# Kernel optimization log

Measured on AMD Instinct MI355X. Metric: run time of the kernel, lower is better.

Reference implementation:

```python
import jax, jax.numpy as jnp
import numpy as np

B, S, D_IN, D_OUT, NUM_LAYERS = 128, 64, 2048, 2048, 64

def setup_inputs() -> dict:
    key = jax.random.key(0)
    k1, k2, k3 = jax.random.split(key, 3)
    x = jax.random.normal(k1, (B, S, D_IN), dtype=jnp.float32)
    weight = jax.random.normal(k2, (NUM_LAYERS, D_OUT, D_IN), dtype=jnp.float32)
    layer_idx = jax.random.randint(k3, (S,), 0, NUM_LAYERS, dtype=jnp.int32)
    return {"x": x, "weight": weight, "layer_idx": layer_idx}

def reference(x, weight, layer_idx):
    # x: [B, S, D_in]; weight: [L, D_out, D_in]; layer_idx: [S] ints in [0, L)
    # Per position s: out[:, s, :] = x[:, s, :] @ weight[layer_idx[s]].T
    w_sel = weight[layer_idx]                      # [S, D_out, D_in] gather
    out = jnp.einsum('bsd,sod->bso', x, w_sel)     # batched per-position GEMMs
    return out
```

## Files before the change

### kernel.cpp

```cpp
#include <hip/hip_runtime.h>
#include <hip/hip_bf16.h>

#define B_DIM 128
#define S_DIM 64
#define DIN   2048
#define DOUT  2048
#define NLAYERS 64

#define BM 128
#define BN 64
#define BK 64
#define NK (DIN / BK)
#define TPP (DOUT / BN)
#define NTILES (S_DIM * TPP)
#define NXCD 8
#define APADE 2048

typedef __bf16 bf16_t;
typedef __attribute__((ext_vector_type(8))) bf16_t bf16x8;
typedef __attribute__((ext_vector_type(4))) float f32x4;

__global__ void rank_sort(const int* __restrict__ layer_idx, int* __restrict__ perm) {
    __shared__ int L[S_DIM];
    const int s = threadIdx.x;
    L[s] = layer_idx[s];
    __syncthreads();
    const int mine = L[s];
    int rank = 0;
    #pragma unroll
    for (int t = 0; t < S_DIM; ++t) {
        const int lt = L[t];
        rank += (lt < mine || (lt == mine && t < s)) ? 1 : 0;
    }
    perm[rank] = s;
}

__global__ void convert_x(const float* __restrict__ x, bf16_t* __restrict__ x16) {
    const size_t i = ((size_t)blockIdx.x * 256 + threadIdx.x) * 8;
    f32x4 a = *(const f32x4*)(x + i);
    f32x4 b = *(const f32x4*)(x + i + 4);
    bf16x8 v;
    #pragma unroll
    for (int j = 0; j < 4; ++j) { v[j] = (bf16_t)a[j]; v[j + 4] = (bf16_t)b[j]; }
    *(bf16x8*)(x16 + i) = v;
}

template <bool XBF16>
__launch_bounds__(256, 2)
__global__ void flex_linear_gemm(const float* __restrict__ x,
                                 const bf16_t* __restrict__ x16,
                                 const float* __restrict__ w,
                                 const int* __restrict__ layer_idx,
                                 const int* __restrict__ perm,
                                 float* __restrict__ out) {
    __shared__ bf16_t Alds[2][BM * BK + APADE];
    __shared__ bf16_t Blds[2][BN * BK];

    const int orig = blockIdx.x;
    const int xcd  = orig & (NXCD - 1);
    const int slot = orig >> 3;
    const int tile = xcd * (NTILES / NXCD) + slot;
    const int yy   = tile / TPP;
    const int nb   = tile % TPP;

    const int s  = perm[yy];
    const int layer = layer_idx[s];

    const float* Bg = w + (size_t)layer * (size_t)(DOUT * DIN) + (size_t)(nb * BN) * DIN;

    const int tid  = threadIdx.x;
    const int lane = tid & 63;
    const int wave = tid >> 6;
    const int wr = (wave >> 1) * 64;
    const int wc = (wave & 1) * 32;
    const int lrow = lane & 15;
    const int lk   = (lane >> 4) * 8;

    int offWA[4], offWB[2];
    const float*  pA[4];
    const bf16_t* pA16[4];
    const float*  pB[2];
    #pragma unroll
    for (int i = 0; i < 4; ++i) {
        const int c   = tid + 256 * i;
        const int row = c >> 3;
        const int kc8 = (c & 7) * 8;
        offWA[i] = (row * BK + kc8) ^ ((row & 7) << 3);
        const size_t aoff = (size_t)row * (S_DIM * DIN) + (size_t)s * DIN + kc8;
        pA[i]   = x   + aoff;
        pA16[i] = x16 + aoff;
    }
    #pragma unroll
    for (int i = 0; i < 2; ++i) {
        const int c   = tid + 256 * i;
        const int row = c >> 3;
        const int kc8 = (c & 7) * 8;
        offWB[i] = (row * BK + kc8) ^ ((row & 7) << 3);
        pB[i] = Bg + (size_t)row * DIN + kc8;
    }
    int offA[2][4], offB[2][2];
    #pragma unroll
    for (int kk = 0; kk < 2; ++kk) {
        #pragma unroll
        for (int m = 0; m < 4; ++m) {
            const int ra = wr + m * 16 + lrow;
            offA[kk][m] = (ra * BK + kk * 32 + lk) ^ ((ra & 7) << 3);
        }
        #pragma unroll
        for (int n = 0; n < 2; ++n) {
            const int rb = wc + n * 16 + lrow;
            offB[kk][n] = (rb * BK + kk * 32 + lk) ^ ((rb & 7) << 3);
        }
    }

    bf16x8 RA16[4];
    f32x4  RA[8];
    f32x4  RB[4];
    f32x4  acc[4][2] = {};

    auto issue = [&](int kb) {
        const int koff = kb * BK;
        #pragma unroll
        for (int i = 0; i < 4; ++i) {
            if constexpr (XBF16) {
                RA16[i] = *(const bf16x8*)(pA16[i] + koff);
            } else {
                const float* a = pA[i] + koff;
                RA[2 * i]     = *(const f32x4*)a;
                RA[2 * i + 1] = *(const f32x4*)(a + 4);
            }
        }
        #pragma unroll
        for (int i = 0; i < 2; ++i) {
            const float* b = pB[i] + koff;
            RB[2 * i]     = *(const f32x4*)b;
            RB[2 * i + 1] = *(const f32x4*)(b + 4);
        }
    };
    auto cvt_write = [&](int buf) {
        bf16_t* Al = &Alds[buf][0];
        bf16_t* Bl = &Blds[buf][0];
        #pragma unroll
        for (int i = 0; i < 4; ++i) {
            if constexpr (XBF16) {
                *(bf16x8*)&Al[offWA[i]] = RA16[i];
            } else {
                bf16x8 va;
                #pragma unroll
                for (int j = 0; j < 4; ++j) {
                    va[j]     = (bf16_t)RA[2 * i][j];
                    va[j + 4] = (bf16_t)RA[2 * i + 1][j];
                }
                *(bf16x8*)&Al[offWA[i]] = va;
            }
        }
        #pragma unroll
        for (int i = 0; i < 2; ++i) {
            bf16x8 vb;
            #pragma unroll
            for (int j = 0; j < 4; ++j) {
                vb[j]     = (bf16_t)RB[2 * i][j];
                vb[j + 4] = (bf16_t)RB[2 * i + 1][j];
            }
            *(bf16x8*)&Bl[offWB[i]] = vb;
        }
    };
    auto compute = [&](int buf) {
        const bf16_t* Al = &Alds[buf][0];
        const bf16_t* Bl = &Blds[buf][0];
        #pragma unroll
        for (int kk = 0; kk < 2; ++kk) {
            bf16x8 af[4], bfr[2];
            #pragma unroll
            for (int m = 0; m < 4; ++m) af[m]  = *(const bf16x8*)&Al[offA[kk][m]];
            #pragma unroll
            for (int n = 0; n < 2; ++n) bfr[n] = *(const bf16x8*)&Bl[offB[kk][n]];
            #pragma unroll
            for (int m = 0; m < 4; ++m)
                #pragma unroll
                for (int n = 0; n < 2; ++n)
                    acc[m][n] = __builtin_amdgcn_mfma_f32_16x16x32_bf16(af[m], bfr[n], acc[m][n], 0, 0, 0);
        }
    };

    issue(0);
    cvt_write(0);
    issue(1);
    for (int kb = 0; kb < NK - 1; ++kb) {
        __syncthreads();
        compute(kb & 1);
        cvt_write((kb + 1) & 1);
        if (kb + 2 < NK) issue(kb + 2);
    }
    __syncthreads();
    compute((NK - 1) & 1);

    float* Og = out + (size_t)s * DOUT + (size_t)(nb * BN);
    #pragma unroll
    for (int m = 0; m < 4; ++m) {
        const int rb = wr + m * 16 + (lane >> 4) * 4;
        #pragma unroll
        for (int r = 0; r < 4; ++r) {
            float* orow = Og + (size_t)(rb + r) * (S_DIM * DOUT);
            #pragma unroll
            for (int n = 0; n < 2; ++n)
                __builtin_nontemporal_store(acc[m][n][r], &orow[wc + n * 16 + (lane & 15)]);
        }
    }
}

extern "C" void kernel_launch(void* const* d_in, const int* in_sizes, int n_in,
                              void* d_out, int out_size, void* d_ws, size_t ws_size,
                              hipStream_t stream) {
    const float* x         = (const float*)d_in[0];
    const float* w         = (const float*)d_in[1];
    const int*   layer_idx = (const int*)d_in[2];
    float*       out       = (float*)d_out;

    int*    perm = (int*)d_ws;
    bf16_t* x16  = (bf16_t*)((char*)d_ws + 512);
    const size_t need = 512 + (size_t)B_DIM * S_DIM * DIN * sizeof(bf16_t);

    rank_sort<<<1, S_DIM, 0, stream>>>(layer_idx, perm);

    if (ws_size >= need) {
        convert_x<<<(B_DIM * S_DIM * DIN / 8) / 256, 256, 0, stream>>>(x, x16);
        flex_linear_gemm<true><<<NTILES, dim3(256), 0, stream>>>(x, x16, w, layer_idx, perm, out);
    } else {
        flex_linear_gemm<false><<<NTILES, dim3(256), 0, stream>>>(x, x16, w, layer_idx, perm, out);
    }
}
```

Baseline: 231.8 us.

## Fuse rank sort into conversion kernel and relax loop barrier to LDS-only wait

Merges the permutation sort into the x-conversion kernel to drop one kernel launch. Replaces __syncthreads in the GEMM main loop with an explicit lgkmcnt wait plus s_barrier, so in-flight global prefetches need not drain at each barrier. The LDS buffers are merged into one array with explicit offsets. The fallback path now runs the conversion kernel into the workspace even when it is too small, which could write out of bounds there.

```diff
diff --git a/kernel.cpp b/kernel.cpp
--- a/kernel.cpp
+++ b/kernel.cpp
@@ -14,28 +14,34 @@
 #define TPP (DOUT / BN)
 #define NTILES (S_DIM * TPP)
 #define NXCD 8
-#define APADE 2048
+
+#define LDS_A 8192
+#define LDS_B 4096
+#define LDS_ELEMS 28672
+#define A_OFF(b) ((b) * LDS_A)
+#define B_OFF(b) (2 * LDS_A + (b) * LDS_B)
 
 typedef __bf16 bf16_t;
 typedef __attribute__((ext_vector_type(8))) bf16_t bf16x8;
 typedef __attribute__((ext_vector_type(4))) float f32x4;
 
-__global__ void rank_sort(const int* __restrict__ layer_idx, int* __restrict__ perm) {
+__global__ void prep(const float* __restrict__ x, bf16_t* __restrict__ x16,
+                     const int* __restrict__ layer_idx, int* __restrict__ perm) {
     __shared__ int L[S_DIM];
-    const int s = threadIdx.x;
-    L[s] = layer_idx[s];
-    __syncthreads();
-    const int mine = L[s];
-    int rank = 0;
-    #pragma unroll
-    for (int t = 0; t < S_DIM; ++t) {
-        const int lt = L[t];
-        rank += (lt < mine || (lt == mine && t < s)) ? 1 : 0;
-    }
-    perm[rank] = s;
-}
-
-__global__ void convert_x(const float* __restrict__ x, bf16_t* __restrict__ x16) {
+    if (blockIdx.x == 0) {
+        if (threadIdx.x < S_DIM) L[threadIdx.x] = layer_idx[threadIdx.x];
+        __syncthreads();
+        if (threadIdx.x < S_DIM) {
+            const int s = threadIdx.x, mine = L[s];
+            int rank = 0;
+            #pragma unroll
+            for (int t = 0; t < S_DIM; ++t) {
+                const int lt = L[t];
+                rank += (lt < mine || (lt == mine && t < s)) ? 1 : 0;
+            }
+            perm[rank] = s;
+        }
+    }
     const size_t i = ((size_t)blockIdx.x * 256 + threadIdx.x) * 8;
     f32x4 a = *(const f32x4*)(x + i);
     f32x4 b = *(const f32x4*)(x + i + 4);
@@ -43,6 +49,14 @@
     #pragma unroll
     for (int j = 0; j < 4; ++j) { v[j] = (bf16_t)a[j]; v[j + 4] = (bf16_t)b[j]; }
     *(bf16x8*)(x16 + i) = v;
+}
+
+__device__ __forceinline__ void lgkm_barrier() {
+    __builtin_amdgcn_sched_barrier(0);
+    asm volatile("s_waitcnt lgkmcnt(0)" ::: "memory");
+    __builtin_amdgcn_sched_barrier(0);
+    __builtin_amdgcn_s_barrier();
+    __builtin_amdgcn_sched_barrier(0);
 }
 
 template <bool XBF16>
@@ -53,15 +67,14 @@
                                  const int* __restrict__ layer_idx,
                                  const int* __restrict__ perm,
                                  float* __restrict__ out) {
-    __shared__ bf16_t Alds[2][BM * BK + APADE];
-    __shared__ bf16_t Blds[2][BN * BK];
+    __shared__ bf16_t lds[LDS_ELEMS];
 
     const int orig = blockIdx.x;
     const int xcd  = orig & (NXCD - 1);
     const int slot = orig >> 3;
     const int tile = xcd * (NTILES / NXCD) + slot;
-    const int yy   = tile / TPP;
-    const int nb   = tile % TPP;
+    const int yy   = tile >> 5;
+    const int nb   = tile & 31;
 
     const int s  = perm[yy];
     const int layer = layer_idx[s];
@@ -138,8 +151,8 @@
         }
     };
     auto cvt_write = [&](int buf) {
-        bf16_t* Al = &Alds[buf][0];
-        bf16_t* Bl = &Blds[buf][0];
+        bf16_t* Al = &lds[A_OFF(buf)];
+        bf16_t* Bl = &lds[B_OFF(buf)];
         #pragma unroll
         for (int i = 0; i < 4; ++i) {
             if constexpr (XBF16) {
@@ -166,8 +179,8 @@
         }
     };
     auto compute = [&](int buf) {
-        const bf16_t* Al = &Alds[buf][0];
-        const bf16_t* Bl = &Blds[buf][0];
+        const bf16_t* Al = &lds[A_OFF(buf)];
+        const bf16_t* Bl = &lds[B_OFF(buf)];
         #pragma unroll
         for (int kk = 0; kk < 2; ++kk) {
             bf16x8 af[4], bfr[2];
@@ -186,14 +199,13 @@
     issue(0);
     cvt_write(0);
     issue(1);
-    for (int kb = 0; kb < NK - 1; ++kb) {
-        __syncthreads();
+    lgkm_barrier();
+    for (int kb = 0; kb < NK; ++kb) {
         compute(kb & 1);
-        cvt_write((kb + 1) & 1);
+        if (kb + 1 < NK) cvt_write((kb + 1) & 1);
         if (kb + 2 < NK) issue(kb + 2);
-    }
-    __syncthreads();
-    compute((NK - 1) & 1);
+        lgkm_barrier();
+    }
 
     float* Og = out + (size_t)s * DOUT + (size_t)(nb * BN);
     #pragma unroll
@@ -221,12 +233,11 @@
     bf16_t* x16  = (bf16_t*)((char*)d_ws + 512);
     const size_t need = 512 + (size_t)B_DIM * S_DIM * DIN * sizeof(bf16_t);
 
-    rank_sort<<<1, S_DIM, 0, stream>>>(layer_idx, perm);
-
     if (ws_size >= need) {
-        convert_x<<<(B_DIM * S_DIM * DIN / 8) / 256, 256, 0, stream>>>(x, x16);
+        prep<<<(B_DIM * S_DIM * DIN / 8) / 256, 256, 0, stream>>>(x, x16, layer_idx, perm);
         flex_linear_gemm<true><<<NTILES, dim3(256), 0, stream>>>(x, x16, w, layer_idx, perm, out);
     } else {
+        prep<<<(B_DIM * S_DIM * DIN / 8) / 256, 256, 0, stream>>>(x, x16, layer_idx, perm);
         flex_linear_gemm<false><<<NTILES, dim3(256), 0, stream>>>(x, x16, w, layer_idx, perm, out);
     }
 }
```

After: 223.8 us. 3.4% less time.
